# Optimization experiments

Measured on AMD Instinct MI355X. Metric: run time of the kernel, lower is better.

The kernel has to match this reference:

```python
import jax, jax.numpy as jnp
import numpy as np


def reference(x, weight, bias):
    """Per-sample dynamic conv2d, expressed as one grouped convolution.

    x:      (B, C_in, H, W)
    weight: (B, C_out, C_in, kH, kW)
    bias:   (B, C_out)
    returns (B, C_out, H_out, W_out) with H_out = H - kH + 1 (valid conv)
    """
    B, C_in, H, W = x.shape
    C_out, kH, kW = weight.shape[1], weight.shape[3], weight.shape[4]
    # Fold batch into channels: groups=B grouped conv == B independent convs.
    x_g = x.reshape(1, B * C_in, H, W)
    w_g = weight.reshape(B * C_out, C_in, kH, kW)
    out = jax.lax.conv_general_dilated(
        x_g, w_g,
        window_strides=(1, 1),
        padding='VALID',
        dimension_numbers=('NCHW', 'OIHW', 'NCHW'),
        feature_group_count=B,
    )  # (1, B*C_out, H_out, W_out)
    out = out.reshape(B, C_out, out.shape[2], out.shape[3])
    return out + bias[:, :, None, None]


def setup_inputs() -> dict:
    key = jax.random.key(0)
    k1, k2, k3 = jax.random.split(key, 3)
    B, C_in, C_out, H, W, kH, kW = 16, 64, 64, 128, 128, 3, 3
    x = jax.random.normal(k1, (B, C_in, H, W), dtype=jnp.float32)
    weight = jax.random.normal(k2, (B, C_out, C_in, kH, kW), dtype=jnp.float32) * 0.05
    bias = jax.random.normal(k3, (B, C_out), dtype=jnp.float32)
    return {"x": x, "weight": weight, "bias": bias}
```

## Files before the change

kernel.cpp:

```cpp
#include <hip/hip_runtime.h>
#include <hip/hip_bf16.h>

#define BATCH 16
#define CI 64
#define CO 64
#define H 128
#define W 128
#define HO 126
#define WO 126

typedef short bfrag __attribute__((ext_vector_type(8)));
typedef float ffrag __attribute__((ext_vector_type(4)));

static __device__ __forceinline__ unsigned short f2bf(float f) {
    unsigned u = __float_as_uint(f);
    u += 0x7fffu + ((u >> 16) & 1u);
    return (unsigned short)(u >> 16);
}

__global__ void wt_prepass(const float* __restrict__ w, unsigned short* __restrict__ w_t) {
    int i = blockIdx.x * 256 + threadIdx.x;
    int ci = i & 63;
    int co = (i >> 6) & 63;
    int bs = i >> 12;
    int b = bs / 9, s = bs - b * 9;
    w_t[i] = f2bf(w[(((b * 64 + co) * 64 + ci) * 9) + s]);
}

__launch_bounds__(256, 2)
__global__ void dynconv_fused(const float* __restrict__ x,
                              const unsigned short* __restrict__ w_t,
                              const float* __restrict__ bias,
                              float* __restrict__ out) {
    __shared__ __align__(16) unsigned short xs[4 * 8192];

    const int tid  = threadIdx.x;
    const int rg   = blockIdx.x;
    const int b    = blockIdx.y;
    const int y0   = rg * 2;
    const int wave = tid >> 6;
    const int lane = tid & 63;
    const int l16  = lane & 15;
    const int lq   = lane >> 4;
    const int wm   = wave & 1;
    const int wn   = wave >> 1;

    {
        const int col = tid & 127;
        const int h   = tid >> 7;
        const float* xb = x + (size_t)b * CI * H * W + (size_t)y0 * W + col;
        #pragma unroll
        for (int row = 0; row < 4; ++row) {
            #pragma unroll
            for (int oc = 0; oc < 4; ++oc) {
                const int o = h * 4 + oc;
                const float* p = xb + (size_t)(o * 8) * (H * W) + row * W;
                unsigned int u[4];
                #pragma unroll
                for (int e = 0; e < 4; ++e) {
                    float f0 = p[(size_t)(2 * e) * (H * W)];
                    float f1 = p[(size_t)(2 * e + 1) * (H * W)];
                    __hip_bfloat162 h2 = __float22bfloat162_rn(make_float2(f0, f1));
                    u[e] = *(unsigned int*)&h2;
                }
                *(uint4*)&xs[(row * 1024 + col * 8 + (o ^ (col & 7))) * 8] = *(const uint4*)u;
            }
        }
    }

    const bfrag* wtb = (const bfrag*)w_t + (size_t)(b * 9) * 512;
    const int co_b = wm * 32 + l16;
    bfrag acur[4], anxt[4];
    #pragma unroll
    for (int ks = 0; ks < 2; ++ks)
        #pragma unroll
        for (int mt = 0; mt < 2; ++mt)
            acur[ks * 2 + mt] = wtb[(co_b + mt * 16) * 8 + ks * 4 + lq];

    ffrag acc[2][8];
    #pragma unroll
    for (int mt = 0; mt < 2; ++mt)
        #pragma unroll
        for (int nt = 0; nt < 8; ++nt)
            acc[mt][nt] = (ffrag){0.f, 0.f, 0.f, 0.f};

    __syncthreads();

    for (int s = 0; s < 9; ++s) {
        if (s < 8) {
            const bfrag* wn2 = wtb + (s + 1) * 512;
            #pragma unroll
            for (int ks = 0; ks < 2; ++ks)
                #pragma unroll
                for (int mt = 0; mt < 2; ++mt)
                    anxt[ks * 2 + mt] = wn2[(co_b + mt * 16) * 8 + ks * 4 + lq];
        }
        const int dy = s / 3, dx = s - dy * 3;
        const int xr = wn + dy;
        #pragma unroll
        for (int ks = 0; ks < 2; ++ks) {
            const int o = ks * 4 + lq;
            #pragma unroll
            for (int nt = 0; nt < 8; ++nt) {
                int colx = nt * 16 + l16 + dx;
                if (colx > 127) colx = 127;
                const bfrag bf = *(const bfrag*)&xs[xr * 8192 + (colx * 8 + (o ^ (colx & 7))) * 8];
                acc[0][nt] = __builtin_amdgcn_mfma_f32_16x16x32_bf16(acur[ks * 2 + 0], bf, acc[0][nt], 0, 0, 0);
                acc[1][nt] = __builtin_amdgcn_mfma_f32_16x16x32_bf16(acur[ks * 2 + 1], bf, acc[1][nt], 0, 0, 0);
            }
        }
        #pragma unroll
        for (int j = 0; j < 4; ++j) acur[j] = anxt[j];
    }

    const int oy = y0 + wn;
    #pragma unroll
    for (int mt = 0; mt < 2; ++mt) {
        #pragma unroll
        for (int r = 0; r < 4; ++r) {
            int co = wm * 32 + mt * 16 + lq * 4 + r;
            float bv = bias[b * 64 + co];
            float* op = out + ((size_t)(b * 64 + co) * HO + oy) * WO;
            #pragma unroll
            for (int nt = 0; nt < 8; ++nt) {
                int ox = nt * 16 + l16;
                if (ox < WO) op[ox] = acc[mt][nt][r] + bv;
            }
        }
    }
}

extern "C" void kernel_launch(void* const* d_in, const int* in_sizes, int n_in,
                              void* d_out, int out_size, void* d_ws, size_t ws_size,
                              hipStream_t stream) {
    const float* x    = (const float*)d_in[0];
    const float* w    = (const float*)d_in[1];
    const float* bias = (const float*)d_in[2];
    float* out        = (float*)d_out;

    unsigned short* w_t = (unsigned short*)d_ws;

    wt_prepass<<<dim3(589824 / 256), dim3(256), 0, stream>>>(w, w_t);
    dynconv_fused<<<dim3(63, BATCH), dim3(256), 0, stream>>>(x, w_t, bias, out);
}
```

Measured before the change: 141.4 us.

## Split output columns into two tiles per block to raise occupancy

Each block now covers 64 output columns instead of 128, with a column-tile grid dimension added. The shared-memory slab shrinks to a 68-column halo tile, the accumulators halve, and launch bounds rise to allow four blocks per CU, giving more blocks and more waves in flight. The cost is a redundant 4-column halo load per tile, twice as many weight-fragment reloads across the grid, and a generic index-decoding loop for staging input.

```diff
diff --git a/kernel.cpp b/kernel.cpp
--- a/kernel.cpp
+++ b/kernel.cpp
@@ -8,6 +8,9 @@
 #define W 128
 #define HO 126
 #define WO 126
+
+#define XC 68
+#define SLAB (XC * 8 * 8)
 
 typedef short bfrag __attribute__((ext_vector_type(8)));
 typedef float ffrag __attribute__((ext_vector_type(4)));
@@ -27,17 +30,19 @@
     w_t[i] = f2bf(w[(((b * 64 + co) * 64 + ci) * 9) + s]);
 }
 
-__launch_bounds__(256, 2)
+__launch_bounds__(256, 4)
 __global__ void dynconv_fused(const float* __restrict__ x,
                               const unsigned short* __restrict__ w_t,
                               const float* __restrict__ bias,
                               float* __restrict__ out) {
-    __shared__ __align__(16) unsigned short xs[4 * 8192];
+    __shared__ __align__(16) unsigned short xs[4 * SLAB];
 
     const int tid  = threadIdx.x;
     const int rg   = blockIdx.x;
-    const int b    = blockIdx.y;
+    const int ct   = blockIdx.y;
+    const int b    = blockIdx.z;
     const int y0   = rg * 2;
+    const int x0   = ct * 64;
     const int wave = tid >> 6;
     const int lane = tid & 63;
     const int l16  = lane & 15;
@@ -46,15 +51,17 @@
     const int wn   = wave >> 1;
 
     {
-        const int col = tid & 127;
-        const int h   = tid >> 7;
-        const float* xb = x + (size_t)b * CI * H * W + (size_t)y0 * W + col;
+        const float* xb = x + (size_t)b * CI * H * W;
         #pragma unroll
-        for (int row = 0; row < 4; ++row) {
-            #pragma unroll
-            for (int oc = 0; oc < 4; ++oc) {
-                const int o = h * 4 + oc;
-                const float* p = xb + (size_t)(o * 8) * (H * W) + row * W;
+        for (int it = 0; it < 9; ++it) {
+            int i = it * 256 + tid;
+            if (i < 4 * 8 * XC) {
+                int row = i / (8 * XC);
+                int rem = i - row * (8 * XC);
+                int o   = rem / XC;
+                int col = rem - o * XC;
+                int gx  = x0 + col; if (gx > 127) gx = 127;
+                const float* p = xb + ((size_t)(o * 8) * H + (y0 + row)) * W + gx;
                 unsigned int u[4];
                 #pragma unroll
                 for (int e = 0; e < 4; ++e) {
@@ -63,7 +70,7 @@
                     __hip_bfloat162 h2 = __float22bfloat162_rn(make_float2(f0, f1));
                     u[e] = *(unsigned int*)&h2;
                 }
-                *(uint4*)&xs[(row * 1024 + col * 8 + (o ^ (col & 7))) * 8] = *(const uint4*)u;
+                *(uint4*)&xs[row * SLAB + (col * 8 + (o ^ (col & 7))) * 8] = *(const uint4*)u;
             }
         }
     }
@@ -77,11 +84,11 @@
         for (int mt = 0; mt < 2; ++mt)
             acur[ks * 2 + mt] = wtb[(co_b + mt * 16) * 8 + ks * 4 + lq];
 
-    ffrag acc[2][8];
+    ffrag acc[2][4];
     #pragma unroll
     for (int mt = 0; mt < 2; ++mt)
         #pragma unroll
-        for (int nt = 0; nt < 8; ++nt)
+        for (int nt = 0; nt < 4; ++nt)
             acc[mt][nt] = (ffrag){0.f, 0.f, 0.f, 0.f};
 
     __syncthreads();
@@ -101,10 +108,9 @@
         for (int ks = 0; ks < 2; ++ks) {
             const int o = ks * 4 + lq;
             #pragma unroll
-            for (int nt = 0; nt < 8; ++nt) {
+            for (int nt = 0; nt < 4; ++nt) {
                 int colx = nt * 16 + l16 + dx;
-                if (colx > 127) colx = 127;
-                const bfrag bf = *(const bfrag*)&xs[xr * 8192 + (colx * 8 + (o ^ (colx & 7))) * 8];
+                const bfrag bf = *(const bfrag*)&xs[xr * SLAB + (colx * 8 + (o ^ (colx & 7))) * 8];
                 acc[0][nt] = __builtin_amdgcn_mfma_f32_16x16x32_bf16(acur[ks * 2 + 0], bf, acc[0][nt], 0, 0, 0);
                 acc[1][nt] = __builtin_amdgcn_mfma_f32_16x16x32_bf16(acur[ks * 2 + 1], bf, acc[1][nt], 0, 0, 0);
             }
@@ -122,8 +128,8 @@
             float bv = bias[b * 64 + co];
             float* op = out + ((size_t)(b * 64 + co) * HO + oy) * WO;
             #pragma unroll
-            for (int nt = 0; nt < 8; ++nt) {
-                int ox = nt * 16 + l16;
+            for (int nt = 0; nt < 4; ++nt) {
+                int ox = x0 + nt * 16 + l16;
                 if (ox < WO) op[ox] = acc[mt][nt][r] + bv;
             }
         }
@@ -141,5 +147,5 @@
     unsigned short* w_t = (unsigned short*)d_ws;
 
     wt_prepass<<<dim3(589824 / 256), dim3(256), 0, stream>>>(w, w_t);
-    dynconv_fused<<<dim3(63, BATCH), dim3(256), 0, stream>>>(x, w_t, bias, out);
+    dynconv_fused<<<dim3(63, 2, BATCH), dim3(256), 0, stream>>>(x, w_t, bias, out);
 }
```

Measured after the change: 161.0 us. +13.9%, slower.
